# Optimization experiments

Hardware: AMD Instinct MI355X
Metric: run time of the kernel (lower is better)

## Reference

```python
import jax, jax.numpy as jnp
import numpy as np

B, T, D, H = 4, 2048, 1024, 16
DK, DV, CHUNK = D // H, 2 * D // H, 64  # head_k_dim=64, head_v_dim=128 (expand_v=2.0)
EPS = 1e-5


def setup_inputs() -> dict:
    key = jax.random.key(0)
    ks = jax.random.split(key, 6)
    s = 0.02
    return {
        "x": jax.random.normal(ks[0], (B, T, D), jnp.float32),
        "Wq": jax.random.normal(ks[1], (D, H * DK), jnp.float32) * s,
        "Wk": jax.random.normal(ks[2], (D, H * DK), jnp.float32) * s,
        "Wv": jax.random.normal(ks[3], (D, H * DV), jnp.float32) * s,
        "Wg": jax.random.normal(ks[4], (D, H * DV), jnp.float32) * s,
        "Wo": jax.random.normal(ks[5], (H * DV, D), jnp.float32) * s,
        "g_norm_w": jnp.ones((DV,), jnp.float32),
    }


def _rope(q):
    # q: [B, T, H, DK]; non-interleaved (rotate-half) rotary, base 10000
    half = DK // 2
    inv_freq = 1.0 / (10000.0 ** (jnp.arange(half, dtype=jnp.float32) / half))
    freqs = jnp.arange(T, dtype=jnp.float32)[:, None] * inv_freq  # [T, half]
    cos = jnp.cos(freqs)[None, :, None, :]
    sin = jnp.sin(freqs)[None, :, None, :]
    q1, q2 = q[..., :half], q[..., half:]
    return jnp.concatenate([q1 * cos - q2 * sin, q2 * cos + q1 * sin], axis=-1)


def reference(x, Wq, Wk, Wv, Wg, Wo, g_norm_w):
    q = _rope((x @ Wq).reshape(B, T, H, DK)) * (DK ** -0.5)
    k = _rope((x @ Wk).reshape(B, T, H, DK))
    v = (x @ Wv).reshape(B, T, H, DV)

    N = T // CHUNK
    def tochunks(t):  # [B,T,H,Dh] -> [N,B,H,C,Dh]
        return t.reshape(B, N, CHUNK, H, t.shape[-1]).transpose(1, 0, 3, 2, 4)
    qc, kc, vc = tochunks(q), tochunks(k), tochunks(v)

    # per-head RetNet decay: gamma_h = 1 - 2^{-5-h}
    gamma = 1.0 - jnp.exp2(-5.0 - jnp.arange(H, dtype=jnp.float32))  # [H]
    i = jnp.arange(CHUNK, dtype=jnp.float32)
    # intra-chunk decay mask D[h,i,j] = gamma^{i-j} for j<=i else 0
    Dmask = jnp.where(i[:, None] >= i[None, :],
                      gamma[:, None, None] ** (i[:, None] - i[None, :]), 0.0)  # [H,C,C]
    cross = gamma[:, None] ** (i + 1.0)          # [H,C] query decay vs prev state
    kdec = gamma[:, None] ** (CHUNK - 1.0 - i)   # [H,C] key decay into new state
    chunk_dec = gamma ** CHUNK                   # [H]

    def step(S, qkv):
        q_, k_, v_ = qkv  # [B,H,C,DK], [B,H,C,DK], [B,H,C,DV]
        attn = jnp.einsum('bhid,bhjd->bhij', q_, k_) * Dmask
        o = jnp.einsum('bhij,bhjv->bhiv', attn, v_)
        o = o + jnp.einsum('bhid,bhdv->bhiv', q_ * cross[None, :, :, None], S)
        S = S * chunk_dec[None, :, None, None] + \
            jnp.einsum('bhjd,bhjv->bhdv', k_ * kdec[None, :, :, None], v_)
        return S, o

    S0 = jnp.zeros((B, H, DK, DV), x.dtype)
    _, o = jax.lax.scan(step, S0, (qc, kc, vc))  # [N,B,H,C,DV]
    o = o.transpose(1, 0, 3, 2, 4).reshape(B, T, H, DV)

    # fused RMSNorm + swish gate (FusedRMSNormSwishGate)
    g = (x @ Wg).reshape(B, T, H, DV)
    o = o * jax.lax.rsqrt(jnp.mean(o * o, axis=-1, keepdims=True) + EPS) * g_norm_w
    o = o * (g * jax.nn.sigmoid(g))
    return o.reshape(B, T, H * DV) @ Wo
```

## Files before the change

### kernel.cpp

```cpp
#include <hip/hip_runtime.h>
#include <hip/hip_bf16.h>
#include <math.h>

typedef unsigned short u16;
typedef unsigned int u32;
typedef __attribute__((ext_vector_type(8))) short bf16x8;
typedef __attribute__((ext_vector_type(4))) float f32x4;


__device__ __forceinline__ u16 f2bf(float f) {
  union { float f; unsigned u; } a; a.f = f;
  unsigned u = a.u;
  unsigned r = (u + 0x7fffu + ((u >> 16) & 1u)) >> 16;
  return (u16)r;
}
__device__ __forceinline__ float bf2f(u16 s) {
  union { unsigned u; float f; } a; a.u = ((unsigned)s) << 16; return a.f;
}

__global__ void k_sentinel(float* out) {
  if (threadIdx.x == 0 && blockIdx.x == 0) out[0] = 1.0e6f;
}

__device__ __forceinline__ void split8r(const float* t, bf16x8& hi, bf16x8& lo) {
#pragma unroll
  for (int m = 0; m < 8; ++m) {
    union { float f; u32 u; } c; c.f = t[m];
    union { u32 u; float f; } hf; hf.u = c.u & 0xffff0000u;
    union { float f; u32 u; } lw; lw.f = t[m] - hf.f;
    hi[m] = (short)(u16)(c.u >> 16);
    lo[m] = (short)(u16)(lw.u >> 16);
  }
}
__device__ __forceinline__ void split8p(const float* __restrict__ p, bf16x8& hi, bf16x8& lo) {
  f32x4 a = *(const f32x4*)p;
  f32x4 b = *(const f32x4*)(p + 4);
  float t[8];
  t[0]=a[0]; t[1]=a[1]; t[2]=a[2]; t[3]=a[3]; t[4]=b[0]; t[5]=b[1]; t[6]=b[2]; t[7]=b[3];
  split8r(t, hi, lo);
}

__device__ __forceinline__ void bar_lds() {
  asm volatile("s_waitcnt lgkmcnt(0)" ::: "memory");
  __builtin_amdgcn_sched_barrier(0);
  __builtin_amdgcn_s_barrier();
}

__device__ __forceinline__ void bar_vm() {
  asm volatile("s_waitcnt vmcnt(0)" ::: "memory");
  __builtin_amdgcn_sched_barrier(0);
  __builtin_amdgcn_s_barrier();
}

__device__ __forceinline__ void gload16(const u16* g, u16* l) {
  __builtin_amdgcn_global_load_lds(
      (const __attribute__((address_space(1))) unsigned int*)g,
      (__attribute__((address_space(3))) unsigned int*)l, 16, 0, 0);
}

__global__ __launch_bounds__(256) void k_cvt_x(const float* __restrict__ src, u16* __restrict__ dst) {
  int i = blockIdx.x * 256 + threadIdx.x;
  float4 v = ((const float4*)src)[i];
  ushort4 o;
  o.x = f2bf(v.x); o.y = f2bf(v.y); o.z = f2bf(v.z); o.w = f2bf(v.w);
  ((ushort4*)dst)[i] = o;
}

__global__ __launch_bounds__(256) void k_ropetab(float2* __restrict__ tab) {
  int idx = blockIdx.x * 256 + threadIdx.x;
  int t = idx >> 5, i = idx & 31;
  float invf = powf(10000.f, -(float)i * (1.f / 32.f));
  float ang = (float)t * invf;
  float2 cs; cs.x = cosf(ang); cs.y = sinf(ang);
  tab[idx] = cs;
}

__global__ __launch_bounds__(256) void k_transpose_all(
    const float* __restrict__ Wq, const float* __restrict__ Wk, const float* __restrict__ Wv,
    const float* __restrict__ Wg, const float* __restrict__ Wo,
    u16* __restrict__ Wqkb, u16* __restrict__ Wvgb, u16* __restrict__ Wob) {
  int z = blockIdx.x;
  const float* src; u16* dst; int K, N, bx, by;
  if (z < 1024)      { src = Wq; dst = Wqkb;                       K = 1024; N = 1024; int r = z;        bx = r & 31; by = r >> 5; }
  else if (z < 2048) { src = Wk; dst = Wqkb + (size_t)1024 * 1024; K = 1024; N = 1024; int r = z - 1024; bx = r & 31; by = r >> 5; }
  else if (z < 4096) { src = Wv; dst = Wvgb;                       K = 1024; N = 2048; int r = z - 2048; bx = r & 63; by = r >> 6; }
  else if (z < 6144) { src = Wg; dst = Wvgb + (size_t)2048 * 1024; K = 1024; N = 2048; int r = z - 4096; bx = r & 63; by = r >> 6; }
  else               { src = Wo; dst = Wob;                        K = 2048; N = 1024; int r = z - 6144; bx = r & 31; by = r >> 5; }
  __shared__ float tile[32][33];
  int n0 = bx * 32, k0 = by * 32;
  int tx = threadIdx.x & 31, ty = threadIdx.x >> 5;
  for (int r = 0; r < 32; r += 8)
    tile[ty + r][tx] = src[(size_t)(k0 + ty + r) * N + n0 + tx];
  __syncthreads();
  for (int r = 0; r < 32; r += 8)
    dst[(size_t)(n0 + ty + r) * K + k0 + tx] = f2bf(tile[tx][ty + r]);
}

__global__ __launch_bounds__(256, 2) void k_gemm_qkvg(const u16* __restrict__ A, const u16* __restrict__ Bt,
                                                      float* __restrict__ qk, u16* __restrict__ vg,
                                                      const float2* __restrict__ tab, int K) {
  __shared__ __attribute__((aligned(16))) u16 As[2][128 * 32];
  __shared__ __attribute__((aligned(16))) u16 Bs[2][128 * 32];
  int id = blockIdx.y * 48 + blockIdx.x;
  int x = id & 7, loc = id >> 3;
  int bxg = loc / 48, rem = loc - bxg * 48;
  int by8 = rem / 6, bxi = rem - by8 * 6;
  int bx = bxg * 6 + bxi, by = x * 8 + by8;
  int i0 = by * 128, n0 = bx * 128;
  int tid = threadIdx.x;
  int lane = tid & 63, w = tid >> 6;
  int wr = (w >> 1) * 64, wc = (w & 1) * 64;
  int srow = lane >> 2, scol = (lane & 3) * 8;
  f32x4 acc[4][4];
#pragma unroll
  for (int m = 0; m < 4; ++m)
#pragma unroll
    for (int n = 0; n < 4; ++n) acc[m][n] = (f32x4){0.f, 0.f, 0.f, 0.f};
  int fr = lane & 15, kb = (lane >> 4) * 8;
  int nkt = K >> 5;

#define STG(t, sl)                                                                   \
  {                                                                                  \
    _Pragma("unroll")                                                                \
    for (int q = 0; q < 2; ++q) {                                                    \
      int s = w * 2 + q;                                                             \
      gload16(&A[(size_t)(i0 + s * 16 + srow) * K + (t) * 32 + scol], &As[sl][s * 512]); \
      gload16(&Bt[(size_t)(n0 + s * 16 + srow) * K + (t) * 32 + scol], &Bs[sl][s * 512]); \
    }                                                                                \
  }

  STG(0, 0);
  bar_vm();
  int cur = 0;
  for (int t = 0; t < nkt; ++t) {
    if (t + 1 < nkt) STG(t + 1, cur ^ 1);
    bf16x8 af[4], bfr[4];
#pragma unroll
    for (int m = 0; m < 4; ++m) af[m] = *(const bf16x8*)&As[cur][(wr + m * 16 + fr) * 32 + kb];
#pragma unroll
    for (int n = 0; n < 4; ++n) bfr[n] = *(const bf16x8*)&Bs[cur][(wc + n * 16 + fr) * 32 + kb];
    __builtin_amdgcn_s_setprio(1);
#pragma unroll
    for (int m = 0; m < 4; ++m)
#pragma unroll
      for (int n = 0; n < 4; ++n)
        acc[m][n] = __builtin_amdgcn_mfma_f32_16x16x32_bf16(af[m], bfr[n], acc[m][n], 0, 0, 0);
    __builtin_amdgcn_s_setprio(0);
    bar_vm();
    cur ^= 1;
  }
#undef STG

  int rb = (lane >> 4) * 4, cb = lane & 15;
  if (n0 < 2048) {
    float scale = (n0 < 1024) ? 0.125f : 1.0f;
#pragma unroll
    for (int m = 0; m < 4; ++m)
#pragma unroll
      for (int n = 0; n < 2; ++n) {
        int gc = n0 + wc + n * 16 + cb;
        int ii = n * 16 + cb;
#pragma unroll
        for (int r = 0; r < 4; ++r) {
          int gr = i0 + wr + m * 16 + rb + r;
          int t = gr & 2047;
          float2 cs = tab[t * 32 + ii];
          float q1 = acc[m][n][r], q2 = acc[m][n + 2][r];
          qk[(size_t)gr * 2048 + gc]      = (q1 * cs.x - q2 * cs.y) * scale;
          qk[(size_t)gr * 2048 + gc + 32] = (q2 * cs.x + q1 * cs.y) * scale;
        }
      }
  } else {
#pragma unroll
    for (int m = 0; m < 4; ++m)
#pragma unroll
      for (int n = 0; n < 4; ++n) {
        int gr = i0 + wr + m * 16 + rb;
        int gc = n0 - 2048 + wc + n * 16 + cb;
#pragma unroll
        for (int r = 0; r < 4; ++r)
          vg[(size_t)(gr + r) * 4096 + gc] = f2bf(acc[m][n][r]);
      }
  }
}

__global__ __launch_bounds__(256, 2) void k_gemm_out(const u16* __restrict__ A, const u16* __restrict__ Bt,
                                                     float* __restrict__ Cv, int N, int K) {
  __shared__ __attribute__((aligned(16))) u16 As[2][128 * 32];
  __shared__ __attribute__((aligned(16))) u16 Bs[2][128 * 32];
  int nbx = gridDim.x;
  int id = blockIdx.y * nbx + blockIdx.x;
  int cpx = (nbx * gridDim.y) >> 3;
  int sw = (id & 7) * cpx + (id >> 3);
  int bx = sw % nbx, by = sw / nbx;
  int i0 = by * 128, n0 = bx * 128;
  int tid = threadIdx.x;
  int lane = tid & 63, w = tid >> 6;
  int wr = (w >> 1) * 64, wc = (w & 1) * 64;
  int srow = lane >> 2, scol = (lane & 3) * 8;
  f32x4 acc[4][4];
#pragma unroll
  for (int m = 0; m < 4; ++m)
#pragma unroll
    for (int n = 0; n < 4; ++n) acc[m][n] = (f32x4){0.f, 0.f, 0.f, 0.f};
  int fr = lane & 15, kb = (lane >> 4) * 8;
  int nkt = K >> 5;

#define STG(t, sl)                                                                   \
  {                                                                                  \
    _Pragma("unroll")                                                                \
    for (int q = 0; q < 2; ++q) {                                                    \
      int s = w * 2 + q;                                                             \
      gload16(&A[(size_t)(i0 + s * 16 + srow) * K + (t) * 32 + scol], &As[sl][s * 512]); \
      gload16(&Bt[(size_t)(n0 + s * 16 + srow) * K + (t) * 32 + scol], &Bs[sl][s * 512]); \
    }                                                                                \
  }

  STG(0, 0);
  bar_vm();
  int cur = 0;
  for (int t = 0; t < nkt; ++t) {
    if (t + 1 < nkt) STG(t + 1, cur ^ 1);
    bf16x8 af[4], bfr[4];
#pragma unroll
    for (int m = 0; m < 4; ++m) af[m] = *(const bf16x8*)&As[cur][(wr + m * 16 + fr) * 32 + kb];
#pragma unroll
    for (int n = 0; n < 4; ++n) bfr[n] = *(const bf16x8*)&Bs[cur][(wc + n * 16 + fr) * 32 + kb];
    __builtin_amdgcn_s_setprio(1);
#pragma unroll
    for (int m = 0; m < 4; ++m)
#pragma unroll
      for (int n = 0; n < 4; ++n)
        acc[m][n] = __builtin_amdgcn_mfma_f32_16x16x32_bf16(af[m], bfr[n], acc[m][n], 0, 0, 0);
    __builtin_amdgcn_s_setprio(0);
    bar_vm();
    cur ^= 1;
  }
#undef STG

  int rb = (lane >> 4) * 4, cb = lane & 15;
#pragma unroll
  for (int m = 0; m < 4; ++m)
#pragma unroll
    for (int n = 0; n < 4; ++n) {
      int gr = i0 + wr + m * 16 + rb;
      int gc = n0 + wc + n * 16 + cb;
#pragma unroll
      for (int r = 0; r < 4; ++r)
        Cv[(size_t)(gr + r) * N + gc] = acc[m][n][r];
    }
}

__global__ __launch_bounds__(512) void k_retention(const float* __restrict__ qk, const u16* __restrict__ vg,
                                                   const float* __restrict__ gnw, u16* __restrict__ og) {
  int bh = blockIdx.x & 63, rq = blockIdx.x >> 6;
  int h = bh & 15, b = bh >> 4;
  int gi0 = rq * 16;

  __shared__ __attribute__((aligned(16))) float qs[16][68];
  __shared__ __attribute__((aligned(16))) float ks[64][68];
  __shared__ __attribute__((aligned(16))) u16 vst[128][88];
  __shared__ __attribute__((aligned(16))) u16 kta_h[8][520];
  __shared__ __attribute__((aligned(16))) u16 kta_l[8][520];
  __shared__ __attribute__((aligned(16))) u16 pa_h[16][68];
  __shared__ __attribute__((aligned(16))) u16 pa_l[16][68];
  __shared__ __attribute__((aligned(16))) u16 sst_h[8][1040];
  __shared__ __attribute__((aligned(16))) u16 sst_l[8][1040];
  __shared__ float dpow[72];
  __shared__ float ssred[8][16];

  int tid = threadIdx.x;
  int w = tid >> 6, l = tid & 63;
  int fr = l & 15, fq = l >> 4;
  float gamma = 1.f - exp2f(-5.f - (float)h);
  if (tid <= 64) dpow[tid] = powf(gamma, (float)tid);
  for (int c = tid; c < 4160; c += 512) { ((u32*)sst_h)[c] = 0; ((u32*)sst_l)[c] = 0; }
  __syncthreads();
  float cdec = dpow[64];

  int e0 = w * 16;
  float gww = gnw[e0 + fr];
  int khmax = (rq < 2) ? 1 : 2;

  int qi = tid >> 4, qd4 = (tid & 15) * 4;
  int sj = tid >> 3, sdg = (tid & 7) * 8;
  int vjp = tid & 31, ve8 = (tid >> 5) * 8;

  f32x4 Sacc[4][2];
#pragma unroll
  for (int dt = 0; dt < 4; ++dt)
#pragma unroll
    for (int nt = 0; nt < 2; ++nt) Sacc[dt][nt] = (f32x4){0.f, 0.f, 0.f, 0.f};

  f32x4 pq = (f32x4){0.f, 0.f, 0.f, 0.f};
  f32x4 pk0, pk1;
  bf16x8 pva, pvb;
  {
    int rowbase = b * 2048;
    if (tid < 256) pq = *(const f32x4*)&qk[(size_t)(rowbase + gi0 + qi) * 2048 + h * 64 + qd4];
    const float* kr = &qk[(size_t)(rowbase + sj) * 2048 + 1024 + h * 64 + sdg];
    pk0 = *(const f32x4*)kr;
    pk1 = *(const f32x4*)(kr + 4);
    const u16* vr = &vg[(size_t)(rowbase + 2 * vjp) * 4096 + h * 128 + ve8];
    pva = *(const bf16x8*)vr;
    pvb = *(const bf16x8*)(vr + 4096);
  }

  for (int n = 0; n < 32; ++n) {
    int rowbase = b * 2048 + n * 64;
    if (tid < 256) *(f32x4*)&qs[qi][qd4] = pq;
    {
      *(f32x4*)&ks[sj][sdg] = pk0;
      *(f32x4*)&ks[sj][sdg + 4] = pk1;
      float kdv = dpow[63 - sj];
      float kd[8];
#pragma unroll
      for (int m = 0; m < 4; ++m) { kd[m] = pk0[m] * kdv; kd[m + 4] = pk1[m] * kdv; }
      bf16x8 kh8, kl8;
      split8r(kd, kh8, kl8);
      int J = sj >> 3, s = sj & 7, dh = tid & 7;
#pragma unroll
      for (int m = 0; m < 8; ++m) {
        int blk = (dh * 8) | (m ^ dh);
        kta_h[J][blk * 8 + s] = (u16)kh8[m];
        kta_l[J][blk * 8 + s] = (u16)kl8[m];
      }
#pragma unroll
      for (int m = 0; m < 8; ++m)
        *(u32*)&vst[ve8 + m][2 * vjp] = (u32)(u16)pva[m] | ((u32)(u16)pvb[m] << 16);
    }
    __syncthreads();
    if (n < 31) {
      int rb2 = rowbase + 64;
      if (tid < 256) pq = *(const f32x4*)&qk[(size_t)(rb2 + gi0 + qi) * 2048 + h * 64 + qd4];
      const float* kr = &qk[(size_t)(rb2 + sj) * 2048 + 1024 + h * 64 + sdg];
      pk0 = *(const f32x4*)kr;
      pk1 = *(const f32x4*)(kr + 4);
      const u16* vr = &vg[(size_t)(rb2 + 2 * vjp) * 4096 + h * 128 + ve8];
      pva = *(const bf16x8*)vr;
      pvb = *(const bf16x8*)(vr + 4096);
    }
    bf16x8 qhc[2], qlc[2];
    split8p(&qs[fr][fq * 8], qhc[0], qlc[0]);
    split8p(&qs[fr][32 + fq * 8], qhc[1], qlc[1]);
    if (w < 4) {
      int ct = w;
      f32x4 at = (f32x4){0.f, 0.f, 0.f, 0.f};
      if (16 * ct <= gi0 + 15) {
#pragma unroll
        for (int kh = 0; kh < 2; ++kh) {
          bf16x8 kbh, kbl;
          split8p(&ks[16 * ct + fr][kh * 32 + fq * 8], kbh, kbl);
          at = __builtin_amdgcn_mfma_f32_16x16x32_bf16(kbh, qhc[kh], at, 0, 0, 0);
          at = __builtin_amdgcn_mfma_f32_16x16x32_bf16(kbl, qhc[kh], at, 0, 0, 0);
          at = __builtin_amdgcn_mfma_f32_16x16x32_bf16(kbh, qlc[kh], at, 0, 0, 0);
        }
      }
      int jb = 16 * ct + fq * 4;
      ushort4 wh, wl;
#pragma unroll
      for (int r = 0; r < 4; ++r) {
        int s = gi0 + fr - (jb + r);
        float val = (s >= 0) ? at[r] * dpow[s] : 0.f;
        union { float f; u32 u; } c; c.f = val;
        union { u32 u; float f; } hf; hf.u = c.u & 0xffff0000u;
        union { float f; u32 u; } lw; lw.f = val - hf.f;
        ((u16*)&wh)[r] = (u16)(c.u >> 16);
        ((u16*)&wl)[r] = (u16)(lw.u >> 16);
      }
      *(ushort4*)&pa_h[fr][jb] = wh;
      *(ushort4*)&pa_l[fr][jb] = wl;
    } else if (n < 31) {
      int eb = (w - 4) * 32;
#pragma unroll
      for (int dt = 0; dt < 4; ++dt)
#pragma unroll
        for (int nt = 0; nt < 2; ++nt)
#pragma unroll
          for (int r = 0; r < 4; ++r) Sacc[dt][nt][r] *= cdec;
      bf16x8 bv[2][2];
#pragma unroll
      for (int kh2 = 0; kh2 < 2; ++kh2)
#pragma unroll
        for (int nt = 0; nt < 2; ++nt)
          bv[kh2][nt] = *(const bf16x8*)&vst[eb + nt * 16 + fr][kh2 * 32 + fq * 8];
#pragma unroll
      for (int kh2 = 0; kh2 < 2; ++kh2) {
#pragma unroll
        for (int dt = 0; dt < 4; ++dt) {
          int d = dt * 16 + fr;
          int blk = d ^ ((dt * 2 + (fr >> 3)) & 7);
          bf16x8 ah = *(const bf16x8*)&kta_h[kh2 * 4 + fq][blk * 8];
          bf16x8 al = *(const bf16x8*)&kta_l[kh2 * 4 + fq][blk * 8];
#pragma unroll
          for (int nt = 0; nt < 2; ++nt) {
            Sacc[dt][nt] = __builtin_amdgcn_mfma_f32_16x16x32_bf16(ah, bv[kh2][nt], Sacc[dt][nt], 0, 0, 0);
            Sacc[dt][nt] = __builtin_amdgcn_mfma_f32_16x16x32_bf16(al, bv[kh2][nt], Sacc[dt][nt], 0, 0, 0);
          }
        }
      }
    }
    bar_lds();
    f32x4 o1 = (f32x4){0.f, 0.f, 0.f, 0.f};
    f32x4 o2 = (f32x4){0.f, 0.f, 0.f, 0.f};
#pragma unroll
    for (int kh2 = 0; kh2 < 2; ++kh2) {
      bf16x8 sh = *(const bf16x8*)&sst_h[kh2 * 4 + fq][(e0 + fr) * 8];
      bf16x8 sl = *(const bf16x8*)&sst_l[kh2 * 4 + fq][(e0 + fr) * 8];
      o2 = __builtin_amdgcn_mfma_f32_16x16x32_bf16(qhc[kh2], sh, o2, 0, 0, 0);
      o2 = __builtin_amdgcn_mfma_f32_16x16x32_bf16(qhc[kh2], sl, o2, 0, 0, 0);
      o2 = __builtin_amdgcn_mfma_f32_16x16x32_bf16(qlc[kh2], sh, o2, 0, 0, 0);
      if (kh2 < khmax) {
        bf16x8 ph = *(const bf16x8*)&pa_h[fr][kh2 * 32 + fq * 8];
        bf16x8 pl = *(const bf16x8*)&pa_l[fr][kh2 * 32 + fq * 8];
        bf16x8 bvv = *(const bf16x8*)&vst[e0 + fr][kh2 * 32 + fq * 8];
        o1 = __builtin_amdgcn_mfma_f32_16x16x32_bf16(ph, bvv, o1, 0, 0, 0);
        o1 = __builtin_amdgcn_mfma_f32_16x16x32_bf16(pl, bvv, o1, 0, 0, 0);
      }
    }
    float ofin[4], ssp[4];
#pragma unroll
    for (int r = 0; r < 4; ++r) {
      int gi = gi0 + fq * 4 + r;
      ofin[r] = o1[r] + dpow[gi + 1] * o2[r];
      ssp[r] = ofin[r] * ofin[r];
    }
#pragma unroll
    for (int r = 0; r < 4; ++r) {
      ssp[r] += __shfl_xor(ssp[r], 1, 64);
      ssp[r] += __shfl_xor(ssp[r], 2, 64);
      ssp[r] += __shfl_xor(ssp[r], 4, 64);
      ssp[r] += __shfl_xor(ssp[r], 8, 64);
    }
    if (fr == 0) {
#pragma unroll
      for (int r = 0; r < 4; ++r) ssred[w][fq * 4 + r] = ssp[r];
    }
    bar_lds();
#pragma unroll
    for (int r = 0; r < 4; ++r) {
      int i16 = fq * 4 + r;
      float tot = 0.f;
#pragma unroll
      for (int w2 = 0; w2 < 8; ++w2) tot += ssred[w2][i16];
      float rms = rsqrtf(tot * (1.f / 128.f) + 1e-5f);
      int grow = rowbase + gi0 + i16;
      float g = bf2f(vg[(size_t)grow * 4096 + 2048 + h * 128 + e0 + fr]);
      float y = ofin[r] * rms * gww * (g / (1.f + expf(-g)));
      og[(size_t)grow * 2048 + h * 128 + e0 + fr] = f2bf(y);
    }
    if (w >= 4 && n < 31) {
      int eb = (w - 4) * 32;
#pragma unroll
      for (int dt = 0; dt < 4; ++dt) {
        int g = dt * 2 + (fq >> 1);
#pragma unroll
        for (int nt = 0; nt < 2; ++nt) {
          int e = eb + nt * 16 + fr;
          ushort4 wh, wl;
#pragma unroll
          for (int r = 0; r < 4; ++r) {
            union { float f; u32 u; } c; c.f = Sacc[dt][nt][r];
            union { u32 u; float f; } hf; hf.u = c.u & 0xffff0000u;
            union { float f; u32 u; } lw; lw.f = Sacc[dt][nt][r] - hf.f;
            ((u16*)&wh)[r] = (u16)(c.u >> 16);
            ((u16*)&wl)[r] = (u16)(lw.u >> 16);
          }
          int idx = e * 8 + (fq & 1) * 4;
          *(ushort4*)&sst_h[g][idx] = wh;
          *(ushort4*)&sst_l[g][idx] = wl;
        }
      }
    }
  }
}

extern "C" void kernel_launch(void* const* d_in, const int* in_sizes, int n_in,
                              void* d_out, int out_size, void* d_ws, size_t ws_size,
                              hipStream_t stream) {
  const float* x   = (const float*)d_in[0];
  const float* Wq  = (const float*)d_in[1];
  const float* Wk  = (const float*)d_in[2];
  const float* Wv  = (const float*)d_in[3];
  const float* Wg  = (const float*)d_in[4];
  const float* Wo  = (const float*)d_in[5];
  const float* gnw = (const float*)d_in[6];
  float* out = (float*)d_out;

  const size_t MB = 1024 * 1024;
  char* ws = (char*)d_ws;
  u16*   xb   = (u16*)(ws + 0 * MB);
  u16*   Wqkb = (u16*)(ws + 16 * MB);
  u16*   Wvgb = (u16*)(ws + 20 * MB);
  float2* tab = (float2*)(ws + 28 * MB);
  float* qk   = (float*)(ws + 32 * MB);
  u16*   vg   = (u16*)(ws + 96 * MB);
  u16*   Wob  = (u16*)(ws + 160 * MB);
  u16*   og   = (u16*)(ws + 0 * MB);
  const size_t NEED = 164 * MB;
  if (ws_size < NEED) {
    k_sentinel<<<1, 64, 0, stream>>>(out);
    return;
  }

  k_cvt_x<<<8192, 256, 0, stream>>>(x, xb);
  k_ropetab<<<256, 256, 0, stream>>>(tab);
  k_transpose_all<<<8192, 256, 0, stream>>>(Wq, Wk, Wv, Wg, Wo, Wqkb, Wvgb, Wob);

  k_gemm_qkvg<<<dim3(48, 64), 256, 0, stream>>>(xb, Wqkb, qk, vg, tab, 1024);
  k_retention<<<256, 512, 0, stream>>>(qk, vg, gnw, og);
  k_gemm_out<<<dim3(8, 64), 256, 0, stream>>>(og, Wob, out, 1024, 2048);
}
```

Baseline: 301.5 us.

## Triple-buffer GEMM LDS stages with swizzled layout and single barrier per k-step

Both bf16 MFMA GEMMs move from double to triple buffering of the A/B LDS tiles. Loads are issued two k-steps ahead, and a partial vmcnt wait lets one stage stay in flight across the barrier. The LDS layout is also XOR-swizzled: the global source addresses are permuted on load and the fragment reads use the matching XOR, aiming to cut bank conflicts on the 16-byte reads. The cost is 50% more LDS per block, which may lower occupancy below the two-blocks-per-CU launch bound, plus extra index arithmetic per load.

```diff
diff --git a/kernel.cpp b/kernel.cpp
--- a/kernel.cpp
+++ b/kernel.cpp
@@ -42,12 +42,6 @@
 
 __device__ __forceinline__ void bar_lds() {
   asm volatile("s_waitcnt lgkmcnt(0)" ::: "memory");
-  __builtin_amdgcn_sched_barrier(0);
-  __builtin_amdgcn_s_barrier();
-}
-
-__device__ __forceinline__ void bar_vm() {
-  asm volatile("s_waitcnt vmcnt(0)" ::: "memory");
   __builtin_amdgcn_sched_barrier(0);
   __builtin_amdgcn_s_barrier();
 }
@@ -96,11 +90,24 @@
     dst[(size_t)(n0 + ty + r) * K + k0 + tx] = f2bf(tile[tx][ty + r]);
 }
 
+#define STG3(t, sl)                                                                  \
+  {                                                                                  \
+    _Pragma("unroll")                                                                \
+    for (int q = 0; q < 2; ++q) {                                                    \
+      int s = w * 2 + q;                                                             \
+      int dByte = s * 1024 + lane * 16;                                              \
+      int u = dByte ^ (((dByte >> 9) & 1) << 5);                                     \
+      int row = u >> 6, cb = u & 63;                                                 \
+      gload16(&A[(size_t)(i0 + row) * K + (t) * 32 + (cb >> 1)], &As[sl][s * 512]);  \
+      gload16(&Bt[(size_t)(n0 + row) * K + (t) * 32 + (cb >> 1)], &Bs[sl][s * 512]); \
+    }                                                                                \
+  }
+
 __global__ __launch_bounds__(256, 2) void k_gemm_qkvg(const u16* __restrict__ A, const u16* __restrict__ Bt,
                                                       float* __restrict__ qk, u16* __restrict__ vg,
                                                       const float2* __restrict__ tab, int K) {
-  __shared__ __attribute__((aligned(16))) u16 As[2][128 * 32];
-  __shared__ __attribute__((aligned(16))) u16 Bs[2][128 * 32];
+  __shared__ __attribute__((aligned(16))) u16 As[3][128 * 32];
+  __shared__ __attribute__((aligned(16))) u16 Bs[3][128 * 32];
   int id = blockIdx.y * 48 + blockIdx.x;
   int x = id & 7, loc = id >> 3;
   int bxg = loc / 48, rem = loc - bxg * 48;
@@ -110,35 +117,37 @@
   int tid = threadIdx.x;
   int lane = tid & 63, w = tid >> 6;
   int wr = (w >> 1) * 64, wc = (w & 1) * 64;
-  int srow = lane >> 2, scol = (lane & 3) * 8;
   f32x4 acc[4][4];
 #pragma unroll
   for (int m = 0; m < 4; ++m)
 #pragma unroll
     for (int n = 0; n < 4; ++n) acc[m][n] = (f32x4){0.f, 0.f, 0.f, 0.f};
-  int fr = lane & 15, kb = (lane >> 4) * 8;
+  int fr = lane & 15, kq = lane >> 4;
   int nkt = K >> 5;
 
-#define STG(t, sl)                                                                   \
-  {                                                                                  \
-    _Pragma("unroll")                                                                \
-    for (int q = 0; q < 2; ++q) {                                                    \
-      int s = w * 2 + q;                                                             \
-      gload16(&A[(size_t)(i0 + s * 16 + srow) * K + (t) * 32 + scol], &As[sl][s * 512]); \
-      gload16(&Bt[(size_t)(n0 + s * 16 + srow) * K + (t) * 32 + scol], &Bs[sl][s * 512]); \
-    }                                                                                \
-  }
-
-  STG(0, 0);
-  bar_vm();
-  int cur = 0;
+  STG3(0, 0);
+  STG3(1, 1);
   for (int t = 0; t < nkt; ++t) {
-    if (t + 1 < nkt) STG(t + 1, cur ^ 1);
+    if (t < nkt - 1) asm volatile("s_waitcnt vmcnt(4)" ::: "memory");
+    else             asm volatile("s_waitcnt vmcnt(0)" ::: "memory");
+    asm volatile("s_waitcnt lgkmcnt(0)" ::: "memory");
+    __builtin_amdgcn_sched_barrier(0);
+    __builtin_amdgcn_s_barrier();
+    if (t + 2 < nkt) STG3(t + 2, (t + 2) % 3);
+    int cur = t % 3;
     bf16x8 af[4], bfr[4];
 #pragma unroll
-    for (int m = 0; m < 4; ++m) af[m] = *(const bf16x8*)&As[cur][(wr + m * 16 + fr) * 32 + kb];
-#pragma unroll
-    for (int n = 0; n < 4; ++n) bfr[n] = *(const bf16x8*)&Bs[cur][(wc + n * 16 + fr) * 32 + kb];
+    for (int m = 0; m < 4; ++m) {
+      int rr = wr + m * 16 + fr;
+      int idx = (rr * 32 + kq * 8) ^ (((rr >> 3) & 1) << 4);
+      af[m] = *(const bf16x8*)&As[cur][idx];
+    }
+#pragma unroll
+    for (int n = 0; n < 4; ++n) {
+      int rr = wc + n * 16 + fr;
+      int idx = (rr * 32 + kq * 8) ^ (((rr >> 3) & 1) << 4);
+      bfr[n] = *(const bf16x8*)&Bs[cur][idx];
+    }
     __builtin_amdgcn_s_setprio(1);
 #pragma unroll
     for (int m = 0; m < 4; ++m)
@@ -146,20 +155,17 @@
       for (int n = 0; n < 4; ++n)
         acc[m][n] = __builtin_amdgcn_mfma_f32_16x16x32_bf16(af[m], bfr[n], acc[m][n], 0, 0, 0);
     __builtin_amdgcn_s_setprio(0);
-    bar_vm();
-    cur ^= 1;
-  }
-#undef STG
-
-  int rb = (lane >> 4) * 4, cb = lane & 15;
+  }
+
+  int rb = (lane >> 4) * 4, cb2 = lane & 15;
   if (n0 < 2048) {
     float scale = (n0 < 1024) ? 0.125f : 1.0f;
 #pragma unroll
     for (int m = 0; m < 4; ++m)
 #pragma unroll
       for (int n = 0; n < 2; ++n) {
-        int gc = n0 + wc + n * 16 + cb;
-        int ii = n * 16 + cb;
+        int gc = n0 + wc + n * 16 + cb2;
+        int ii = n * 16 + cb2;
 #pragma unroll
         for (int r = 0; r < 4; ++r) {
           int gr = i0 + wr + m * 16 + rb + r;
@@ -176,7 +182,7 @@
 #pragma unroll
       for (int n = 0; n < 4; ++n) {
         int gr = i0 + wr + m * 16 + rb;
-        int gc = n0 - 2048 + wc + n * 16 + cb;
+        int gc = n0 - 2048 + wc + n * 16 + cb2;
 #pragma unroll
         for (int r = 0; r < 4; ++r)
           vg[(size_t)(gr + r) * 4096 + gc] = f2bf(acc[m][n][r]);
@@ -186,8 +192,8 @@
 
 __global__ __launch_bounds__(256, 2) void k_gemm_out(const u16* __restrict__ A, const u16* __restrict__ Bt,
                                                      float* __restrict__ Cv, int N, int K) {
-  __shared__ __attribute__((aligned(16))) u16 As[2][128 * 32];
-  __shared__ __attribute__((aligned(16))) u16 Bs[2][128 * 32];
+  __shared__ __attribute__((aligned(16))) u16 As[3][128 * 32];
+  __shared__ __attribute__((aligned(16))) u16 Bs[3][128 * 32];
   int nbx = gridDim.x;
   int id = blockIdx.y * nbx + blockIdx.x;
   int cpx = (nbx * gridDim.y) >> 3;
@@ -197,35 +203,37 @@
   int tid = threadIdx.x;
   int lane = tid & 63, w = tid >> 6;
   int wr = (w >> 1) * 64, wc = (w & 1) * 64;
-  int srow = lane >> 2, scol = (lane & 3) * 8;
   f32x4 acc[4][4];
 #pragma unroll
   for (int m = 0; m < 4; ++m)
 #pragma unroll
     for (int n = 0; n < 4; ++n) acc[m][n] = (f32x4){0.f, 0.f, 0.f, 0.f};
-  int fr = lane & 15, kb = (lane >> 4) * 8;
+  int fr = lane & 15, kq = lane >> 4;
   int nkt = K >> 5;
 
-#define STG(t, sl)                                                                   \
-  {                                                                                  \
-    _Pragma("unroll")                                                                \
-    for (int q = 0; q < 2; ++q) {                                                    \
-      int s = w * 2 + q;                                                             \
-      gload16(&A[(size_t)(i0 + s * 16 + srow) * K + (t) * 32 + scol], &As[sl][s * 512]); \
-      gload16(&Bt[(size_t)(n0 + s * 16 + srow) * K + (t) * 32 + scol], &Bs[sl][s * 512]); \
-    }                                                                                \
-  }
-
-  STG(0, 0);
-  bar_vm();
-  int cur = 0;
+  STG3(0, 0);
+  STG3(1, 1);
   for (int t = 0; t < nkt; ++t) {
-    if (t + 1 < nkt) STG(t + 1, cur ^ 1);
+    if (t < nkt - 1) asm volatile("s_waitcnt vmcnt(4)" ::: "memory");
+    else             asm volatile("s_waitcnt vmcnt(0)" ::: "memory");
+    asm volatile("s_waitcnt lgkmcnt(0)" ::: "memory");
+    __builtin_amdgcn_sched_barrier(0);
+    __builtin_amdgcn_s_barrier();
+    if (t + 2 < nkt) STG3(t + 2, (t + 2) % 3);
+    int cur = t % 3;
     bf16x8 af[4], bfr[4];
 #pragma unroll
-    for (int m = 0; m < 4; ++m) af[m] = *(const bf16x8*)&As[cur][(wr + m * 16 + fr) * 32 + kb];
-#pragma unroll
-    for (int n = 0; n < 4; ++n) bfr[n] = *(const bf16x8*)&Bs[cur][(wc + n * 16 + fr) * 32 + kb];
+    for (int m = 0; m < 4; ++m) {
+      int rr = wr + m * 16 + fr;
+      int idx = (rr * 32 + kq * 8) ^ (((rr >> 3) & 1) << 4);
+      af[m] = *(const bf16x8*)&As[cur][idx];
+    }
+#pragma unroll
+    for (int n = 0; n < 4; ++n) {
+      int rr = wc + n * 16 + fr;
+      int idx = (rr * 32 + kq * 8) ^ (((rr >> 3) & 1) << 4);
+      bfr[n] = *(const bf16x8*)&Bs[cur][idx];
+    }
     __builtin_amdgcn_s_setprio(1);
 #pragma unroll
     for (int m = 0; m < 4; ++m)
@@ -233,18 +241,15 @@
       for (int n = 0; n < 4; ++n)
         acc[m][n] = __builtin_amdgcn_mfma_f32_16x16x32_bf16(af[m], bfr[n], acc[m][n], 0, 0, 0);
     __builtin_amdgcn_s_setprio(0);
-    bar_vm();
-    cur ^= 1;
-  }
-#undef STG
-
-  int rb = (lane >> 4) * 4, cb = lane & 15;
+  }
+
+  int rb = (lane >> 4) * 4, cb2 = lane & 15;
 #pragma unroll
   for (int m = 0; m < 4; ++m)
 #pragma unroll
     for (int n = 0; n < 4; ++n) {
       int gr = i0 + wr + m * 16 + rb;
-      int gc = n0 + wc + n * 16 + cb;
+      int gc = n0 + wc + n * 16 + cb2;
 #pragma unroll
       for (int r = 0; r < 4; ++r)
         Cv[(size_t)(gr + r) * N + gc] = acc[m][n][r];
```

Result: no change. 299.9 us, median of 2 (-0.5%).
